# Performance work log

Hardware: AMD Instinct MI355X
Metric: run time of the kernel (lower is better)

Reference implementation:

```python
import jax, jax.numpy as jnp
import numpy as np

M_TOKENS, D_IN, D_OUT = 4096, 4096, 16384


def setup_inputs() -> dict:
    key = jax.random.key(0)
    k1, k2, k3, k4 = jax.random.split(key, 4)
    x = jax.random.normal(k1, (M_TOKENS, D_IN), dtype=jnp.float32)
    # pre-quantized int8 weight, stored [K, N] as in qweight_kn
    qweight_kn = jax.random.randint(k2, (D_IN, D_OUT), -127, 128, dtype=jnp.int8)
    # per-output-channel weight dequant scales (float16 buffer, used as fp32 in kernel)
    weight_scales = jax.random.uniform(k3, (D_OUT,), dtype=jnp.float32, minval=1e-3, maxval=2e-2)
    bias = jax.random.normal(k4, (D_OUT,), dtype=jnp.float32) * 0.01
    return {"x": x, "qweight_kn": qweight_kn, "weight_scales": weight_scales, "bias": bias}


def reference(x, qweight_kn, weight_scales, bias):
    target_dtype = x.dtype
    x2 = x.reshape(-1, x.shape[-1])  # [M, K]
    # dynamic per-token (per-row) symmetric quantization
    x_max = jnp.max(jnp.abs(x2), axis=-1, keepdims=True).astype(jnp.float32) + 1e-5
    x_scales = x_max / 127.0  # [M, 1]
    x_int8 = jnp.clip(jnp.round(x2.astype(jnp.float32) / x_scales), -128, 127).astype(jnp.int8)
    acc = jax.lax.dot_general(
        x_int8, qweight_kn,
        dimension_numbers=(((1,), (0,)), ((), ())),
        preferred_element_type=jnp.int32,
    )  # [M, N] int32
    # fused dequant: row act-scale * col weight-scale, plus bias
    c = acc.astype(jnp.float32) * x_scales * weight_scales[None, :].astype(jnp.float32)
    c = c + bias[None, :]
    out = c.astype(jnp.bfloat16)  # kernel stores bf16
    return out.reshape(*x.shape[:-1], -1).astype(target_dtype)
```

## Files before the change

### kernel.cpp

```cpp
#include <hip/hip_runtime.h>
#include <hip/hip_bf16.h>
#include <stdint.h>

typedef int v4i __attribute__((ext_vector_type(4)));

#define BM 128
#define BN 128
#define BK 64
#define LDS_STRIDE 80

__global__ __launch_bounds__(256) void quant_rows(
    const float* __restrict__ x, int8_t* __restrict__ xq,
    float* __restrict__ xs, int K) {
  const int row = blockIdx.x;
  const int t = threadIdx.x;
  const float4* src = (const float4*)(x + (size_t)row * K) + t * 4;
  float4 v[4];
  float m = 0.f;
#pragma unroll
  for (int i = 0; i < 4; ++i) {
    v[i] = src[i];
    m = fmaxf(m, fmaxf(fmaxf(fabsf(v[i].x), fabsf(v[i].y)),
                       fmaxf(fabsf(v[i].z), fabsf(v[i].w))));
  }
#pragma unroll
  for (int off = 1; off < 64; off <<= 1)
    m = fmaxf(m, __shfl_xor(m, off, 64));
  __shared__ float wmax[4];
  if ((t & 63) == 0) wmax[t >> 6] = m;
  __syncthreads();
  const float gm = fmaxf(fmaxf(wmax[0], wmax[1]), fmaxf(wmax[2], wmax[3]));
  const float scale = (gm + 1e-5f) / 127.0f;
  if (t == 0) xs[row] = scale;
  unsigned packed[4];
#pragma unroll
  for (int i = 0; i < 4; ++i) {
    float fv[4] = {v[i].x, v[i].y, v[i].z, v[i].w};
    unsigned p = 0;
#pragma unroll
    for (int j = 0; j < 4; ++j) {
      int q = (int)rintf(fv[j] / scale);
      q = max(-128, min(127, q));
      p |= (unsigned)(q & 0xff) << (8 * j);
    }
    packed[i] = p;
  }
  *(int4*)(xq + (size_t)row * K + t * 16) =
      make_int4((int)packed[0], (int)packed[1], (int)packed[2], (int)packed[3]);
}

__global__ __launch_bounds__(256) void transpose_pack(
    const int* __restrict__ W32, int8_t* __restrict__ Wt, int K, int N) {
  __shared__ __align__(16) int8_t tile[64][LDS_STRIDE];
  const int t = threadIdx.x;
  const int n0 = blockIdx.x * 64;
  const int k0 = blockIdx.y * 64;
  const int ln = t & 63;
  const int wv = t >> 6;
#pragma unroll
  for (int it = 0; it < 16; ++it) {
    const int kk = wv * 16 + it;
    tile[ln][kk] = (int8_t)W32[(size_t)(k0 + kk) * N + n0 + ln];
  }
  __syncthreads();
  const int kb = wv * 16;
  const int4 v = *(const int4*)&tile[ln][kb];
  *(int4*)(Wt + (size_t)(n0 + ln) * K + k0 + kb) = v;
}

__global__ __launch_bounds__(256) void gemm_i8(
    const int8_t* __restrict__ Xq, const int8_t* __restrict__ Wt,
    const float* __restrict__ xs, const float* __restrict__ wsc,
    const float* __restrict__ bias, float* __restrict__ C,
    int M, int N, int K) {
  __shared__ __align__(16) int8_t lA[2][BM * LDS_STRIDE];
  __shared__ __align__(16) int8_t lB[2][BN * LDS_STRIDE];
  const int t = threadIdx.x;
  const int lane = t & 63;
  const int wid = t >> 6;
  const size_t rowA0 = (size_t)blockIdx.y * BM;
  const size_t rowB0 = (size_t)blockIdx.x * BN;
  const int NT = K / BK;

  const int r0 = t >> 2, kb = (t & 3) * 16;
  const int8_t* gA0 = Xq + (rowA0 + r0) * K + kb;
  const int8_t* gA1 = gA0 + (size_t)64 * K;
  const int8_t* gB0 = Wt + (rowB0 + r0) * K + kb;
  const int8_t* gB1 = gB0 + (size_t)64 * K;
  const int oS0 = r0 * LDS_STRIDE + kb;
  const int oS1 = oS0 + 64 * LDS_STRIDE;

  {
    int4 a0 = *(const int4*)gA0, a1 = *(const int4*)gA1;
    int4 b0 = *(const int4*)gB0, b1 = *(const int4*)gB1;
    *(int4*)&lA[0][oS0] = a0;
    *(int4*)&lA[0][oS1] = a1;
    *(int4*)&lB[0][oS0] = b0;
    *(int4*)&lB[0][oS1] = b1;
  }
  __syncthreads();

  v4i acc[4][4] = {};
  const int wr = wid >> 1, wc = wid & 1;
  const int fr = lane & 15;
  const int ks = (lane >> 4) * 16;

  for (int kt = 0; kt < NT; ++kt) {
    const int cur = kt & 1;
    int4 a0, a1, b0, b1;
    if (kt + 1 < NT) {
      const size_t ko = (size_t)(kt + 1) * BK;
      a0 = *(const int4*)(gA0 + ko);
      a1 = *(const int4*)(gA1 + ko);
      b0 = *(const int4*)(gB0 + ko);
      b1 = *(const int4*)(gB1 + ko);
    }
    v4i af[4], bf[4];
#pragma unroll
    for (int i = 0; i < 4; ++i) {
      af[i] = *(const v4i*)&lA[cur][(wr * 64 + i * 16 + fr) * LDS_STRIDE + ks];
      bf[i] = *(const v4i*)&lB[cur][(wc * 64 + i * 16 + fr) * LDS_STRIDE + ks];
    }
#pragma unroll
    for (int i = 0; i < 4; ++i)
#pragma unroll
      for (int j = 0; j < 4; ++j)
        acc[i][j] =
            __builtin_amdgcn_mfma_i32_16x16x64_i8(af[i], bf[j], acc[i][j], 0, 0, 0);
    if (kt + 1 < NT) {
      const int nb = cur ^ 1;
      *(int4*)&lA[nb][oS0] = a0;
      *(int4*)&lA[nb][oS1] = a1;
      *(int4*)&lB[nb][oS0] = b0;
      *(int4*)&lB[nb][oS1] = b1;
      __syncthreads();
    }
  }

#pragma unroll
  for (int i = 0; i < 4; ++i) {
    const int row_l = wr * 64 + i * 16 + (lane >> 4) * 4;
#pragma unroll
    for (int r = 0; r < 4; ++r) {
      const size_t row = rowA0 + row_l + r;
      const float xv = xs[row];
      float* crow = C + row * (size_t)N + rowB0;
#pragma unroll
      for (int j = 0; j < 4; ++j) {
        const int col_l = wc * 64 + j * 16 + fr;
        const float f =
            (float)acc[i][j][r] * xv * wsc[rowB0 + col_l] + bias[rowB0 + col_l];
        crow[col_l] = __bfloat162float(__float2bfloat16(f));
      }
    }
  }
}

extern "C" void kernel_launch(void* const* d_in, const int* in_sizes, int n_in,
                              void* d_out, int out_size, void* d_ws, size_t ws_size,
                              hipStream_t stream) {
  const int M = 4096, K = 4096, N = 16384;
  const float* x = (const float*)d_in[0];
  const int* W32 = (const int*)d_in[1];
  const float* wsc = (const float*)d_in[2];
  const float* bias = (const float*)d_in[3];
  float* out = (float*)d_out;

  float* xs = (float*)d_ws;
  int8_t* Xq = (int8_t*)d_ws + 16384;
  int8_t* Wt = (int8_t*)d_ws + 16384 + (size_t)M * K;

  transpose_pack<<<dim3(N / 64, K / 64), 256, 0, stream>>>(W32, Wt, K, N);
  quant_rows<<<M, 256, 0, stream>>>(x, Xq, xs, K);
  gemm_i8<<<dim3(N / BN, M / BM), 256, 0, stream>>>(Xq, Wt, xs, wsc, bias, out, M,
                                                    N, K);
}
```

Before: 484.2 us.

## Rewrite int8 GEMM with 256x256 tiles, direct-to-LDS loads and XCD-aware scheduling

Replaces the GEMM kernel with a 512-thread, 256x256x128 tile design. Global tiles go straight into XOR-swizzled LDS through global_load_lds, with two stages kept in flight. MFMA work is split into phases around barriers and setprio, and block IDs are remapped so each XCD gets a contiguous group of N tiles. The aim is more data reuse per block, no register round-trip or bank conflicts on the LDS path, and better L2 locality. In exchange it uses much more LDS and registers, which lowers occupancy, and hardcodes the problem dimensions.

```diff
diff --git a/kernel.cpp b/kernel.cpp
--- a/kernel.cpp
+++ b/kernel.cpp
@@ -4,10 +4,19 @@
 
 typedef int v4i __attribute__((ext_vector_type(4)));
 
-#define BM 128
-#define BN 128
-#define BK 64
-#define LDS_STRIDE 80
+#define GM 4096
+#define GN 16384
+#define GK 4096
+#define BM 256
+#define BN 256
+#define BK 128
+#define NTILES (GK / BK)
+
+__device__ __forceinline__ void gload16(const void* g, void* l) {
+  __builtin_amdgcn_global_load_lds(
+      (const __attribute__((address_space(1))) void*)g,
+      (__attribute__((address_space(3))) void*)l, 16, 0, 0);
+}
 
 __global__ __launch_bounds__(256) void quant_rows(
     const float* __restrict__ x, int8_t* __restrict__ xq,
@@ -51,7 +60,7 @@
 
 __global__ __launch_bounds__(256) void transpose_pack(
     const int* __restrict__ W32, int8_t* __restrict__ Wt, int K, int N) {
-  __shared__ __align__(16) int8_t tile[64][LDS_STRIDE];
+  __shared__ __align__(16) int8_t tile[64][80];
   const int t = threadIdx.x;
   const int n0 = blockIdx.x * 64;
   const int k0 = blockIdx.y * 64;
@@ -68,89 +77,137 @@
   *(int4*)(Wt + (size_t)(n0 + ln) * K + k0 + kb) = v;
 }
 
-__global__ __launch_bounds__(256) void gemm_i8(
+__global__ __launch_bounds__(512, 2) void gemm_i8(
     const int8_t* __restrict__ Xq, const int8_t* __restrict__ Wt,
     const float* __restrict__ xs, const float* __restrict__ wsc,
-    const float* __restrict__ bias, float* __restrict__ C,
-    int M, int N, int K) {
-  __shared__ __align__(16) int8_t lA[2][BM * LDS_STRIDE];
-  __shared__ __align__(16) int8_t lB[2][BN * LDS_STRIDE];
+    const float* __restrict__ bias, float* __restrict__ C) {
+  __shared__ __align__(16) int8_t lA[2][BM][BK];
+  __shared__ __align__(16) int8_t lB[2][BN][BK];
+
   const int t = threadIdx.x;
   const int lane = t & 63;
-  const int wid = t >> 6;
-  const size_t rowA0 = (size_t)blockIdx.y * BM;
-  const size_t rowB0 = (size_t)blockIdx.x * BN;
-  const int NT = K / BK;
-
-  const int r0 = t >> 2, kb = (t & 3) * 16;
-  const int8_t* gA0 = Xq + (rowA0 + r0) * K + kb;
-  const int8_t* gA1 = gA0 + (size_t)64 * K;
-  const int8_t* gB0 = Wt + (rowB0 + r0) * K + kb;
-  const int8_t* gB1 = gB0 + (size_t)64 * K;
-  const int oS0 = r0 * LDS_STRIDE + kb;
-  const int oS1 = oS0 + 64 * LDS_STRIDE;
-
-  {
-    int4 a0 = *(const int4*)gA0, a1 = *(const int4*)gA1;
-    int4 b0 = *(const int4*)gB0, b1 = *(const int4*)gB1;
-    *(int4*)&lA[0][oS0] = a0;
-    *(int4*)&lA[0][oS1] = a1;
-    *(int4*)&lB[0][oS0] = b0;
-    *(int4*)&lB[0][oS1] = b1;
-  }
-  __syncthreads();
-
-  v4i acc[4][4] = {};
-  const int wr = wid >> 1, wc = wid & 1;
+  const int w = t >> 6;
+  const int wr = w >> 2;
+  const int wc = w & 3;
   const int fr = lane & 15;
-  const int ks = (lane >> 4) * 16;
-
-  for (int kt = 0; kt < NT; ++kt) {
-    const int cur = kt & 1;
-    int4 a0, a1, b0, b1;
-    if (kt + 1 < NT) {
-      const size_t ko = (size_t)(kt + 1) * BK;
-      a0 = *(const int4*)(gA0 + ko);
-      a1 = *(const int4*)(gA1 + ko);
-      b0 = *(const int4*)(gB0 + ko);
-      b1 = *(const int4*)(gB1 + ko);
+  const int kg = lane >> 4;
+
+  const int bid = blockIdx.x;
+  const int xcd = bid & 7;
+  const int q = bid >> 3;
+  const int tm = q & 15;
+  const int tn = xcd * 8 + (q >> 4);
+  const size_t rowA0 = (size_t)tm * BM;
+  const size_t rowB0 = (size_t)tn * BN;
+
+  const int8_t* XqB = Xq + rowA0 * GK;
+  const int8_t* WtB = Wt + rowB0 * GK;
+  int srcOff[4], dstOff[4];
+#pragma unroll
+  for (int i = 0; i < 4; ++i) {
+    const int slot0 = (i * 8 + w) * 64;
+    const int slot = slot0 + lane;
+    const int r = slot >> 3;
+    const int c = (slot & 7) ^ (r & 7);
+    srcOff[i] = r * GK + c * 16;
+    dstOff[i] = slot0 * 16;
+  }
+
+#define STAGE(KT, D)                                                       \
+  {                                                                        \
+    const int ko = (KT)*BK;                                                \
+    _Pragma("unroll") for (int i = 0; i < 4; ++i)                          \
+        gload16(XqB + srcOff[i] + ko, (int8_t*)&lA[(D)][0][0] + dstOff[i]);\
+    _Pragma("unroll") for (int i = 0; i < 4; ++i)                          \
+        gload16(WtB + srcOff[i] + ko, (int8_t*)&lB[(D)][0][0] + dstOff[i]);\
+  }
+
+  const int ck0 = (((0 * 4) + kg) ^ (fr & 7)) * 16;
+  const int ck1 = (((1 * 4) + kg) ^ (fr & 7)) * 16;
+
+#define LDA_ROW(DSTI, MI, D)                                        \
+  {                                                                 \
+    const int8_t* p = &lA[(D)][wr * 128 + (MI)*16 + fr][0];         \
+    areg[DSTI][0] = *(const v4i*)(p + ck0);                         \
+    areg[DSTI][1] = *(const v4i*)(p + ck1);                         \
+  }
+#define LDB_ROW(NJ, D)                                              \
+  {                                                                 \
+    const int8_t* p = &lB[(D)][wc * 64 + (NJ)*16 + fr][0];          \
+    breg[NJ][0] = *(const v4i*)(p + ck0);                           \
+    breg[NJ][1] = *(const v4i*)(p + ck1);                           \
+  }
+
+#define MFMA_QUAD(MI0, NJ0)                                                    \
+  _Pragma("unroll") for (int mi = 0; mi < 4; ++mi)                             \
+      _Pragma("unroll") for (int nj = 0; nj < 2; ++nj) {                       \
+    acc[(MI0) + mi][(NJ0) + nj] = __builtin_amdgcn_mfma_i32_16x16x64_i8(       \
+        areg[mi][0], breg[(NJ0) + nj][0], acc[(MI0) + mi][(NJ0) + nj], 0, 0, 0);\
+    acc[(MI0) + mi][(NJ0) + nj] = __builtin_amdgcn_mfma_i32_16x16x64_i8(       \
+        areg[mi][1], breg[(NJ0) + nj][1], acc[(MI0) + mi][(NJ0) + nj], 0, 0, 0);\
+  }
+
+#define PHASE_TAIL(MI0, NJ0)                                 \
+  __builtin_amdgcn_s_barrier();                              \
+  asm volatile("s_waitcnt lgkmcnt(0)" ::: "memory");         \
+  __builtin_amdgcn_sched_barrier(0);                         \
+  __builtin_amdgcn_s_setprio(1);                             \
+  MFMA_QUAD(MI0, NJ0);                                       \
+  __builtin_amdgcn_s_setprio(0);                             \
+  __builtin_amdgcn_s_barrier();
+
+  STAGE(0, 0);
+  STAGE(1, 1);
+  asm volatile("s_waitcnt vmcnt(8)" ::: "memory");
+  __builtin_amdgcn_s_barrier();
+
+  v4i acc[8][4] = {};
+  v4i areg[4][2], breg[4][2];
+
+  for (int kt = 0; kt < NTILES; ++kt) {
+    const int d = kt & 1;
+#pragma unroll
+    for (int mi = 0; mi < 4; ++mi) LDA_ROW(mi, mi, d);
+    LDB_ROW(0, d);
+    LDB_ROW(1, d);
+    PHASE_TAIL(0, 0);
+    LDB_ROW(2, d);
+    LDB_ROW(3, d);
+    PHASE_TAIL(0, 2);
+#pragma unroll
+    for (int mi = 0; mi < 4; ++mi) LDA_ROW(mi, mi + 4, d);
+    PHASE_TAIL(4, 0);
+    if (kt + 2 < NTILES) STAGE(kt + 2, d);
+    __builtin_amdgcn_s_barrier();
+    __builtin_amdgcn_s_setprio(1);
+    MFMA_QUAD(4, 2);
+    __builtin_amdgcn_s_setprio(0);
+    if (kt + 2 < NTILES) {
+      asm volatile("s_waitcnt vmcnt(8)" ::: "memory");
+    } else {
+      asm volatile("s_waitcnt vmcnt(0)" ::: "memory");
     }
-    v4i af[4], bf[4];
-#pragma unroll
-    for (int i = 0; i < 4; ++i) {
-      af[i] = *(const v4i*)&lA[cur][(wr * 64 + i * 16 + fr) * LDS_STRIDE + ks];
-      bf[i] = *(const v4i*)&lB[cur][(wc * 64 + i * 16 + fr) * LDS_STRIDE + ks];
-    }
-#pragma unroll
-    for (int i = 0; i < 4; ++i)
-#pragma unroll
-      for (int j = 0; j < 4; ++j)
-        acc[i][j] =
-            __builtin_amdgcn_mfma_i32_16x16x64_i8(af[i], bf[j], acc[i][j], 0, 0, 0);
-    if (kt + 1 < NT) {
-      const int nb = cur ^ 1;
-      *(int4*)&lA[nb][oS0] = a0;
-      *(int4*)&lA[nb][oS1] = a1;
-      *(int4*)&lB[nb][oS0] = b0;
-      *(int4*)&lB[nb][oS1] = b1;
-      __syncthreads();
-    }
-  }
-
-#pragma unroll
-  for (int i = 0; i < 4; ++i) {
-    const int row_l = wr * 64 + i * 16 + (lane >> 4) * 4;
-#pragma unroll
-    for (int r = 0; r < 4; ++r) {
-      const size_t row = rowA0 + row_l + r;
-      const float xv = xs[row];
-      float* crow = C + row * (size_t)N + rowB0;
-#pragma unroll
-      for (int j = 0; j < 4; ++j) {
-        const int col_l = wc * 64 + j * 16 + fr;
-        const float f =
-            (float)acc[i][j][r] * xv * wsc[rowB0 + col_l] + bias[rowB0 + col_l];
-        crow[col_l] = __bfloat162float(__float2bfloat16(f));
+    __builtin_amdgcn_s_barrier();
+  }
+
+  float xsv[8][4];
+#pragma unroll
+  for (int mi = 0; mi < 8; ++mi)
+#pragma unroll
+    for (int r = 0; r < 4; ++r)
+      xsv[mi][r] = xs[rowA0 + wr * 128 + mi * 16 + kg * 4 + r];
+#pragma unroll
+  for (int nj = 0; nj < 4; ++nj) {
+    const int col_l = wc * 64 + nj * 16 + fr;
+    const float wsv = wsc[rowB0 + col_l];
+    const float bv = bias[rowB0 + col_l];
+#pragma unroll
+    for (int mi = 0; mi < 8; ++mi) {
+#pragma unroll
+      for (int r = 0; r < 4; ++r) {
+        const size_t row = rowA0 + wr * 128 + mi * 16 + kg * 4 + r;
+        const float f = (float)acc[mi][nj][r] * xsv[mi][r] * wsv + bv;
+        C[row * GN + rowB0 + col_l] = __bfloat162float(__float2bfloat16(f));
       }
     }
   }
@@ -159,7 +216,7 @@
 extern "C" void kernel_launch(void* const* d_in, const int* in_sizes, int n_in,
                               void* d_out, int out_size, void* d_ws, size_t ws_size,
                               hipStream_t stream) {
-  const int M = 4096, K = 4096, N = 16384;
+  const int M = GM, K = GK, N = GN;
   const float* x = (const float*)d_in[0];
   const int* W32 = (const int*)d_in[1];
   const float* wsc = (const float*)d_in[2];
@@ -172,6 +229,6 @@
 
   transpose_pack<<<dim3(N / 64, K / 64), 256, 0, stream>>>(W32, Wt, K, N);
   quant_rows<<<M, 256, 0, stream>>>(x, Xq, xs, K);
-  gemm_i8<<<dim3(N / BN, M / BM), 256, 0, stream>>>(Xq, Wt, xs, wsc, bias, out, M,
-                                                    N, K);
-}
+  gemm_i8<<<dim3((M / BM) * (N / BN)), 512, 0, stream>>>(Xq, Wt, xs, wsc, bias,
+                                                         out);
+}
```

Measured after the change: 494.3 us. 2.1% more time.
